# Kernel optimization log

Hardware: AMD Instinct MI355X
Metric: run time of the kernel (lower is better)

## Reference

```python
import jax, jax.numpy as jnp
import numpy as np

B, S, D_IN, D_OUT = 4, 2048, 1024, 1024


def setup_inputs() -> dict:
    key = jax.random.key(0)
    k1, k2, k3, k4 = jax.random.split(key, 4)
    x = jax.random.normal(k1, (B, S, D_IN), dtype=jnp.float32)
    # torch nn.Linear weight layout: [d_out, d_in]
    wq = jax.random.normal(k2, (D_OUT, D_IN), dtype=jnp.float32) * (1.0 / np.sqrt(D_IN))
    wk = jax.random.normal(k3, (D_OUT, D_IN), dtype=jnp.float32) * (1.0 / np.sqrt(D_IN))
    wv = jax.random.normal(k4, (D_OUT, D_IN), dtype=jnp.float32) * (1.0 / np.sqrt(D_IN))
    return {"x": x, "wq": wq, "wk": wk, "wv": wv}


def reference(x, wq, wk, wv):
    # q,k,v: [b, s, d_out]
    q = jnp.einsum('bsd,od->bso', x, wq)
    k = jnp.einsum('bsd,od->bso', x, wk)
    v = jnp.einsum('bsd,od->bso', x, wv)
    scale = 1.0 / jnp.sqrt(jnp.asarray(k.shape[-1], dtype=q.dtype))
    scores = jnp.einsum('bqd,bkd->bqk', q, k)  # [b, s, s]
    s = scores.shape[-1]
    causal = jnp.tril(jnp.ones((s, s), dtype=bool))
    scores = jnp.where(causal, scores, -jnp.inf)
    attn = jax.nn.softmax(scores * scale, axis=-1)
    # dropout p=0.0 -> identity
    return jnp.einsum('bqk,bkd->bqd', attn, v)
```

## Files before the change

### kernel.cpp

```cpp
#include <hip/hip_runtime.h>
#include <hip/hip_bf16.h>
#include <cstdint>

#define BATCH 4
#define SEQ   2048
#define DIN   1024
#define DOUT  1024
#define SCALE 0.03125f

typedef unsigned short u16;
typedef float  f32x4  __attribute__((ext_vector_type(4)));
typedef __bf16 bf16x8 __attribute__((ext_vector_type(8)));

__device__ __forceinline__ u16 f2bf(float f) {
    unsigned u = __float_as_uint(f);
    unsigned r = 0x7fffu + ((u >> 16) & 1u);
    return (u16)((u + r) >> 16);
}

__device__ __forceinline__ f32x4 mfma16(bf16x8 a, bf16x8 b, f32x4 c) {
    return __builtin_amdgcn_mfma_f32_16x16x32_bf16(a, b, c, 0, 0, 0);
}

__device__ __forceinline__ void gl_lds16(const u16* g, u16* l) {
    __builtin_amdgcn_global_load_lds(
        (const __attribute__((address_space(1))) unsigned int*)g,
        (__attribute__((address_space(3))) unsigned int*)l, 16, 0, 0);
}

#define BAR    asm volatile("s_barrier" ::: "memory")
#define VMCNT3 asm volatile("s_waitcnt vmcnt(3)" ::: "memory")
#define VMCNT8 asm volatile("s_waitcnt vmcnt(8)" ::: "memory")
#define VMCNT0 asm volatile("s_waitcnt vmcnt(0)" ::: "memory")
#define LGKM0  asm volatile("s_waitcnt lgkmcnt(0)" ::: "memory")

__global__ __launch_bounds__(256) void cvt_all(const float* __restrict__ x,
                                               const float* __restrict__ wq,
                                               const float* __restrict__ wk,
                                               const float* __restrict__ wv,
                                               u16* __restrict__ dst,
                                               float* __restrict__ rowsum) {
    const size_t NX = (size_t)BATCH * SEQ * DIN;
    size_t gt = (size_t)blockIdx.x * 256 + threadIdx.x;
    if (gt < 1024) {
        f32x4 z = {0.f, 0.f, 0.f, 0.f};
        *(f32x4*)(rowsum + gt * 8) = z;
        *(f32x4*)(rowsum + gt * 8 + 4) = z;
    }
    size_t e = gt * 8;
    const float* src;
    size_t off;
    if (e < NX) { src = x; off = e; }
    else {
        size_t r = e - NX;
        int w = (int)(r >> 20);
        src = (w == 0) ? wq : (w == 1) ? wk : wv;
        off = r & ((1u << 20) - 1);
    }
    f32x4 a = *(const f32x4*)(src + off);
    f32x4 b = *(const f32x4*)(src + off + 4);
    uint4 o;
    o.x = (unsigned)f2bf(a[0]) | ((unsigned)f2bf(a[1]) << 16);
    o.y = (unsigned)f2bf(a[2]) | ((unsigned)f2bf(a[3]) << 16);
    o.z = (unsigned)f2bf(b[0]) | ((unsigned)f2bf(b[1]) << 16);
    o.w = (unsigned)f2bf(b[2]) | ((unsigned)f2bf(b[3]) << 16);
    *(uint4*)(dst + e) = o;
}

__device__ __forceinline__ void stg128(const u16* __restrict__ g, int ld,
                                       u16* unit, int tid) {
#pragma unroll
    for (int i = 0; i < 2; i++) {
        int D = (i * 512 + tid) * 16;
        int r = D >> 7, w = D & 127;
        int gcol = (w ^ ((r & 7) << 4)) >> 1;
        gl_lds16(g + (size_t)r * ld + gcol, unit + (i * 512 + (tid >> 6) * 64) * 8);
    }
}

__device__ __forceinline__ void stg192(const u16* __restrict__ g, int ld,
                                       u16* unit, int tid) {
#pragma unroll
    for (int i = 0; i < 3; i++) {
        int D = (i * 512 + tid) * 16;
        int r = D >> 7, w = D & 127;
        int gcol = (w ^ ((r & 7) << 4)) >> 1;
        gl_lds16(g + (size_t)r * ld + gcol, unit + (i * 512 + (tid >> 6) * 64) * 8);
    }
}

__device__ __forceinline__ void stg4(const u16* __restrict__ g, int ld,
                                     u16* unit, int tid) {
#pragma unroll
    for (int i = 0; i < 4; i++) {
        int D = (i * 256 + tid) * 16;
        int r = D >> 7, w = D & 127;
        int gcol = (w ^ ((r & 7) << 4)) >> 1;
        gl_lds16(g + (size_t)r * ld + gcol, unit + (i * 256 + (tid >> 6) * 64) * 8);
    }
}

__device__ __forceinline__ void rd4(const u16* unit, int rowbase, int l15, int l4,
                                    bf16x8 f[4][2]) {
    const char* u = (const char*)unit;
#pragma unroll
    for (int i = 0; i < 4; i++) {
        int row = rowbase + i * 16 + l15;
#pragma unroll
        for (int kk = 0; kk < 2; kk++)
            f[i][kk] = *(const bf16x8*)(u + row * 128 +
                                        ((kk * 64 + l4 * 16) ^ ((row & 7) << 4)));
    }
}

__device__ __forceinline__ void rd3(const u16* unit, int rowbase, int l15, int l4,
                                    bf16x8 f[3][2]) {
    const char* u = (const char*)unit;
#pragma unroll
    for (int i = 0; i < 3; i++) {
        int row = rowbase + i * 16 + l15;
#pragma unroll
        for (int kk = 0; kk < 2; kk++)
            f[i][kk] = *(const bf16x8*)(u + row * 128 +
                                        ((kk * 64 + l4 * 16) ^ ((row & 7) << 4)));
    }
}

__device__ __forceinline__ void g4_body(u16* lds, const u16* __restrict__ Ag,
                                        int lda, const u16* __restrict__ Bg,
                                        int ldb, int nkt, int wm, int wn,
                                        int l15, int l4, int tid,
                                        f32x4 acc[4][4]) {
    bf16x8 a[4][2], b[4][2];
    u16* A0 = lds;          u16* B0 = lds + 8192;
    u16* A1 = lds + 16384;  u16* B1 = lds + 24576;
    stg4(Ag, lda, A0, tid);      stg4(Bg, ldb, B0, tid);
    stg4(Ag + 64, lda, A1, tid); stg4(Bg + 64, ldb, B1, tid);
    VMCNT8; BAR;
    for (int t = 0; t < nkt; t += 2) {
        {
            const int k2 = ((t + 2 < nkt) ? t + 2 : nkt - 1) * 64;
            rd4(A0, wm * 64, l15, l4, a);
            rd4(B0, wn * 64, l15, l4, b);
            BAR;
            __builtin_amdgcn_s_setprio(1);
#pragma unroll
            for (int kk = 0; kk < 2; kk++)
#pragma unroll
                for (int mi = 0; mi < 4; mi++)
#pragma unroll
                    for (int ni = 0; ni < 2; ni++)
                        acc[mi][ni] = mfma16(a[mi][kk], b[ni][kk], acc[mi][ni]);
            __builtin_amdgcn_s_setprio(0);
            LGKM0; BAR;
            stg4(Ag + k2, lda, A0, tid);
            stg4(Bg + k2, ldb, B0, tid);
            VMCNT8; BAR;
            __builtin_amdgcn_s_setprio(1);
#pragma unroll
            for (int kk = 0; kk < 2; kk++)
#pragma unroll
                for (int mi = 0; mi < 4; mi++)
#pragma unroll
                    for (int ni = 2; ni < 4; ni++)
                        acc[mi][ni] = mfma16(a[mi][kk], b[ni][kk], acc[mi][ni]);
            __builtin_amdgcn_s_setprio(0);
            BAR;
        }
        {
            const int k3 = ((t + 3 < nkt) ? t + 3 : nkt - 1) * 64;
            rd4(A1, wm * 64, l15, l4, a);
            rd4(B1, wn * 64, l15, l4, b);
            BAR;
            __builtin_amdgcn_s_setprio(1);
#pragma unroll
            for (int kk = 0; kk < 2; kk++)
#pragma unroll
                for (int mi = 0; mi < 4; mi++)
#pragma unroll
                    for (int ni = 0; ni < 2; ni++)
                        acc[mi][ni] = mfma16(a[mi][kk], b[ni][kk], acc[mi][ni]);
            __builtin_amdgcn_s_setprio(0);
            LGKM0; BAR;
            stg4(Ag + k3, lda, A1, tid);
            stg4(Bg + k3, ldb, B1, tid);
            VMCNT8; BAR;
            __builtin_amdgcn_s_setprio(1);
#pragma unroll
            for (int kk = 0; kk < 2; kk++)
#pragma unroll
                for (int mi = 0; mi < 4; mi++)
#pragma unroll
                    for (int ni = 2; ni < 4; ni++)
                        acc[mi][ni] = mfma16(a[mi][kk], b[ni][kk], acc[mi][ni]);
            __builtin_amdgcn_s_setprio(0);
            BAR;
        }
    }
    VMCNT0;
}

#define QKV_PH0(AU, BU, ANX0, ANX1, K1)                                      \
    rd4((AU), 0, l15, l4, a);                                                \
    rd3((BU), wn * 48, l15, l4, b);                                          \
    stg128(Ag + (K1), DIN, (ANX0), tid);                                     \
    stg128(Ag + (size_t)128 * DIN + (K1), DIN, (ANX1), tid);                 \
    BAR;                                                                     \
    __builtin_amdgcn_s_setprio(1);                                           \
    _Pragma("unroll") for (int kk = 0; kk < 2; kk++)                         \
    _Pragma("unroll") for (int mi = 0; mi < 4; mi++)                         \
    _Pragma("unroll") for (int ni = 0; ni < 3; ni++)                         \
        acc[mi][ni] = mfma16(a[mi][kk], b[ni][kk], acc[mi][ni]);             \
    __builtin_amdgcn_s_setprio(0);                                           \
    BAR;

#define QKV_PH1(AU, BCUR, K2)                                                \
    rd4((AU), 64, l15, l4, a);                                               \
    stg192(Bg + (K2), DIN, (BCUR), tid);                                     \
    VMCNT3; BAR;                                                             \
    __builtin_amdgcn_s_setprio(1);                                           \
    _Pragma("unroll") for (int kk = 0; kk < 2; kk++)                         \
    _Pragma("unroll") for (int mi = 0; mi < 4; mi++)                         \
    _Pragma("unroll") for (int ni = 0; ni < 3; ni++)                         \
        acc[4 + mi][ni] = mfma16(a[mi][kk], b[ni][kk], acc[4 + mi][ni]);     \
    __builtin_amdgcn_s_setprio(0);                                           \
    BAR;

__global__ __launch_bounds__(512) void qkv_gemm192(const u16* __restrict__ xb,
                                                   const u16* __restrict__ wb,
                                                   u16* __restrict__ qkv,
                                                   u16* __restrict__ vt) {
    extern __shared__ __align__(16) u16 lds[];
    const int tid = threadIdx.x, lane = tid & 63, wid = tid >> 6;
    const int wm = wid >> 2, wn = wid & 3;
    const int l15 = lane & 15, l4 = lane >> 4;

    u16* A00 = lds;          u16* A01 = lds + 8192;
    u16* A10 = lds + 16384;  u16* A11 = lds + 24576;
    u16* B0  = lds + 32768;  u16* B1  = lds + 45056;
    u16* Ar0 = lds + wm * 8192;
    u16* Ar1 = lds + 16384 + wm * 8192;

    for (int tile = blockIdx.x; tile < 512; tile += 256) {
        const int wg = (tile & 7) * 64 + (tile >> 3);
        const int mt = wg & 31, nt = wg >> 5;
        const int m0 = mt * 256, n0 = nt * 192;
        const u16* Ag = xb + (size_t)m0 * DIN;
        const u16* Bg = wb + (size_t)n0 * DIN;
        f32x4 acc[8][3] = {};
        bf16x8 a[4][2], b[3][2];

        stg128(Ag, DIN, A00, tid);
        stg128(Ag + (size_t)128 * DIN, DIN, A01, tid);
        stg192(Bg, DIN, B0, tid);
        stg192(Bg + 64, DIN, B1, tid);
        VMCNT3;
        BAR;

        for (int i = 0; i < 8; i++) {
            const int k1 = (2 * i + 1) * 64;
            const int k2 = ((2 * i + 2 < 16) ? 2 * i + 2 : 15) * 64;
            const int k3 = ((2 * i + 3 < 16) ? 2 * i + 3 : 15) * 64;
            QKV_PH0(Ar0, B0, A10, A11, k1)
            QKV_PH1(Ar0, B0, k2)
            QKV_PH0(Ar1, B1, A00, A01, k2)
            QKV_PH1(Ar1, B1, k3)
        }
        VMCNT0;

#pragma unroll
        for (int ai = 0; ai < 8; ai++)
#pragma unroll
            for (int bj = 0; bj < 3; bj++) {
                const int colb = n0 + wn * 48 + bj * 16;
                const int row = m0 + wm * 128 + ai * 16 + l4 * 4;
                if (colb >= 2 * DOUT) {
                    int d = colb + l15 - 2 * DOUT;
                    int batch = row >> 11, s0 = row & 2047;
                    uint2 o;
                    o.x = (unsigned)f2bf(acc[ai][bj][0]) |
                          ((unsigned)f2bf(acc[ai][bj][1]) << 16);
                    o.y = (unsigned)f2bf(acc[ai][bj][2]) |
                          ((unsigned)f2bf(acc[ai][bj][3]) << 16);
                    *(uint2*)&vt[(size_t)batch * DOUT * SEQ + (size_t)d * SEQ + s0] = o;
                } else {
                    const int wsel = colb >> 10;
                    u16* Op = qkv + (size_t)wsel * ((size_t)BATCH * SEQ * DOUT);
                    const int col = (colb & 1023) + l15;
#pragma unroll
                    for (int rr = 0; rr < 4; rr++)
                        Op[(size_t)(row + rr) * DOUT + col] = f2bf(acc[ai][bj][rr]);
                }
            }
    }
}

__global__ __launch_bounds__(256) void qk4(const u16* __restrict__ qg,
                                           const u16* __restrict__ kg,
                                           u16* __restrict__ sg,
                                           float* __restrict__ rowsum) {
    extern __shared__ __align__(16) u16 lds[];
    const int bxx = blockIdx.x, batch = blockIdx.y;
    int mt = 0, base = 0;
#pragma unroll 16
    for (int m = 0; m < 16; m++) {
        int c = m + 1;
        if (bxx < base + c) { mt = m; break; }
        base += c;
    }
    const int nt = bxx - base;
    const int m0 = mt * 128, n0 = nt * 128;
    const int tid = threadIdx.x, lane = tid & 63, wid = tid >> 6;
    const int wm = wid >> 1, wn = wid & 1;
    const int l15 = lane & 15, l4 = lane >> 4;
    const size_t bo = (size_t)batch * SEQ * DOUT;

    f32x4 acc[4][4] = {};
    g4_body(lds, qg + bo + (size_t)m0 * DOUT, DOUT,
            kg + bo + (size_t)n0 * DOUT, DOUT, 16,
            wm, wn, l15, l4, tid, acc);

    u16* Sp = sg + (size_t)batch * SEQ * SEQ;
    float* Rs = rowsum + (size_t)batch * SEQ;
#pragma unroll
    for (int ai = 0; ai < 4; ai++)
#pragma unroll
        for (int rr = 0; rr < 4; rr++) {
            int q = m0 + wm * 64 + ai * 16 + l4 * 4 + rr;
            float rp = 0.f;
#pragma unroll
            for (int bj = 0; bj < 4; bj++) {
                int kc = n0 + wn * 64 + bj * 16 + l15;
                float p = (kc <= q) ? __expf(acc[ai][bj][rr] * SCALE) : 0.f;
                rp += p;
                Sp[(size_t)q * SEQ + kc] = f2bf(p);
            }
#pragma unroll
            for (int off = 8; off >= 1; off >>= 1) rp += __shfl_xor(rp, off, 16);
            if (l15 == 0) atomicAdd(&Rs[q], rp);
        }
}

__global__ __launch_bounds__(256) void pv4(const u16* __restrict__ pg,
                                           const u16* __restrict__ vtg,
                                           const float* __restrict__ rowsum,
                                           float* __restrict__ og) {
    extern __shared__ __align__(16) u16 lds[];
    const int mt = (blockIdx.z < 2) ? (15 - (int)blockIdx.x) : (int)blockIdx.x;
    const int n0 = blockIdx.y * 128, batch = blockIdx.z;
    const int m0 = mt * 128;
    const int nkt = (mt + 1) * 2;
    const int tid = threadIdx.x, lane = tid & 63, wid = tid >> 6;
    const int wm = wid >> 1, wn = wid & 1;
    const int l15 = lane & 15, l4 = lane >> 4;
    const u16* Pb = pg + (size_t)batch * SEQ * SEQ;
    const u16* Vb = vtg + (size_t)batch * DOUT * SEQ + (size_t)n0 * SEQ;
    const float* Rs = rowsum + (size_t)batch * SEQ;
    float* Ob = og + (size_t)batch * SEQ * DOUT;

    f32x4 acc[4][4] = {};
    g4_body(lds, Pb + (size_t)m0 * SEQ, SEQ, Vb, SEQ, nkt,
            wm, wn, l15, l4, tid, acc);

#pragma unroll
    for (int ai = 0; ai < 4; ai++)
#pragma unroll
        for (int rr = 0; rr < 4; rr++) {
            int q = m0 + wm * 64 + ai * 16 + l4 * 4 + rr;
            float inv = 1.0f / Rs[q];
#pragma unroll
            for (int bj = 0; bj < 4; bj++) {
                int d = n0 + wn * 64 + bj * 16 + l15;
                Ob[(size_t)q * DOUT + d] = acc[ai][bj][rr] * inv;
            }
        }
}

extern "C" void kernel_launch(void* const* d_in, const int* in_sizes, int n_in,
                              void* d_out, int out_size, void* d_ws, size_t ws_size,
                              hipStream_t stream) {
    const float* x  = (const float*)d_in[0];
    const float* wq = (const float*)d_in[1];
    const float* wk = (const float*)d_in[2];
    const float* wv = (const float*)d_in[3];
    float* out = (float*)d_out;

    const size_t NX  = (size_t)BATCH * SEQ * DIN;
    const size_t NWT = (size_t)DOUT * DIN;
    u16* xb  = (u16*)d_ws;
    u16* wb  = xb + NX;
    u16* qkv = wb + 3 * NWT;
    u16* vt  = qkv + 3 * NX;
    u16* sb  = vt + NX;
    float* rowsum = (float*)(sb + (size_t)BATCH * SEQ * SEQ);

    cvt_all<<<(NX + 3 * NWT) / 8 / 256, 256, 0, stream>>>(x, wq, wk, wv, xb, rowsum);

    (void)hipFuncSetAttribute((const void*)qkv_gemm192,
                              hipFuncAttributeMaxDynamicSharedMemorySize, 114688);
    (void)hipFuncSetAttribute((const void*)qk4,
                              hipFuncAttributeMaxDynamicSharedMemorySize, 65536);
    (void)hipFuncSetAttribute((const void*)pv4,
                              hipFuncAttributeMaxDynamicSharedMemorySize, 65536);

    qkv_gemm192<<<dim3(256), dim3(512), 114688, stream>>>(xb, wb, qkv, vt);

    qk4<<<dim3(136, BATCH), dim3(256), 65536, stream>>>(qkv, qkv + NX, sb, rowsum);

    pv4<<<dim3(16, 8, 4), dim3(256), 65536, stream>>>(sb, vt, rowsum, out);
}
```

Baseline: 147.6 us.

## Replace 512-thread 256x192 QKV GEMM with 256-thread 128x192 double-buffered tiles

Swaps the QKV projection kernel from 512-thread workgroups computing 256x192 tiles (with split A/B staging phases) for 256-thread workgroups computing 128x192 tiles. The new kernel uses a simple two-stage double buffer over K in 80 KB of LDS, and each wave holds a 64x96 accumulator. The smaller LDS footprint and smaller blocks may let more workgroups share a CU and give finer load balance. The cost is less operand reuse per tile and a somewhat different load/compute overlap schedule.

```diff
diff --git a/kernel.cpp b/kernel.cpp
--- a/kernel.cpp
+++ b/kernel.cpp
@@ -28,11 +28,11 @@
         (__attribute__((address_space(3))) unsigned int*)l, 16, 0, 0);
 }
 
-#define BAR    asm volatile("s_barrier" ::: "memory")
-#define VMCNT3 asm volatile("s_waitcnt vmcnt(3)" ::: "memory")
-#define VMCNT8 asm volatile("s_waitcnt vmcnt(8)" ::: "memory")
-#define VMCNT0 asm volatile("s_waitcnt vmcnt(0)" ::: "memory")
-#define LGKM0  asm volatile("s_waitcnt lgkmcnt(0)" ::: "memory")
+#define BAR     asm volatile("s_barrier" ::: "memory")
+#define VMCNT8  asm volatile("s_waitcnt vmcnt(8)" ::: "memory")
+#define VMCNT10 asm volatile("s_waitcnt vmcnt(10)" ::: "memory")
+#define VMCNT0  asm volatile("s_waitcnt vmcnt(0)" ::: "memory")
+#define LGKM0   asm volatile("s_waitcnt lgkmcnt(0)" ::: "memory")
 
 __global__ __launch_bounds__(256) void cvt_all(const float* __restrict__ x,
                                                const float* __restrict__ wq,
@@ -67,32 +67,21 @@
     *(uint4*)(dst + e) = o;
 }
 
-__device__ __forceinline__ void stg128(const u16* __restrict__ g, int ld,
-                                       u16* unit, int tid) {
-#pragma unroll
-    for (int i = 0; i < 2; i++) {
-        int D = (i * 512 + tid) * 16;
+__device__ __forceinline__ void stg4(const u16* __restrict__ g, int ld,
+                                     u16* unit, int tid) {
+#pragma unroll
+    for (int i = 0; i < 4; i++) {
+        int D = (i * 256 + tid) * 16;
         int r = D >> 7, w = D & 127;
         int gcol = (w ^ ((r & 7) << 4)) >> 1;
-        gl_lds16(g + (size_t)r * ld + gcol, unit + (i * 512 + (tid >> 6) * 64) * 8);
-    }
-}
-
-__device__ __forceinline__ void stg192(const u16* __restrict__ g, int ld,
-                                       u16* unit, int tid) {
-#pragma unroll
-    for (int i = 0; i < 3; i++) {
-        int D = (i * 512 + tid) * 16;
-        int r = D >> 7, w = D & 127;
-        int gcol = (w ^ ((r & 7) << 4)) >> 1;
-        gl_lds16(g + (size_t)r * ld + gcol, unit + (i * 512 + (tid >> 6) * 64) * 8);
-    }
-}
-
-__device__ __forceinline__ void stg4(const u16* __restrict__ g, int ld,
+        gl_lds16(g + (size_t)r * ld + gcol, unit + (i * 256 + (tid >> 6) * 64) * 8);
+    }
+}
+
+__device__ __forceinline__ void stg6(const u16* __restrict__ g, int ld,
                                      u16* unit, int tid) {
 #pragma unroll
-    for (int i = 0; i < 4; i++) {
+    for (int i = 0; i < 6; i++) {
         int D = (i * 256 + tid) * 16;
         int r = D >> 7, w = D & 127;
         int gcol = (w ^ ((r & 7) << 4)) >> 1;
@@ -200,11 +189,10 @@
     VMCNT0;
 }
 
-#define QKV_PH0(AU, BU, ANX0, ANX1, K1)                                      \
-    rd4((AU), 0, l15, l4, a);                                                \
-    rd3((BU), wn * 48, l15, l4, b);                                          \
-    stg128(Ag + (K1), DIN, (ANX0), tid);                                     \
-    stg128(Ag + (size_t)128 * DIN + (K1), DIN, (ANX1), tid);                 \
+#define QKV4_TILE(AC, BC, KN)                                                \
+    rd4((AC), wm * 64, l15, l4, a);                                          \
+    rd3((BC), wn * 96, l15, l4, b);                                          \
+    rd3((BC), wn * 96 + 48, l15, l4, b + 3);                                 \
     BAR;                                                                     \
     __builtin_amdgcn_s_setprio(1);                                           \
     _Pragma("unroll") for (int kk = 0; kk < 2; kk++)                         \
@@ -212,68 +200,57 @@
     _Pragma("unroll") for (int ni = 0; ni < 3; ni++)                         \
         acc[mi][ni] = mfma16(a[mi][kk], b[ni][kk], acc[mi][ni]);             \
     __builtin_amdgcn_s_setprio(0);                                           \
-    BAR;
-
-#define QKV_PH1(AU, BCUR, K2)                                                \
-    rd4((AU), 64, l15, l4, a);                                               \
-    stg192(Bg + (K2), DIN, (BCUR), tid);                                     \
-    VMCNT3; BAR;                                                             \
+    LGKM0; BAR;                                                              \
+    stg4(Ag + (KN), DIN, (AC), tid);                                         \
+    stg6(Bg + (KN), DIN, (BC), tid);                                         \
+    VMCNT10; BAR;                                                            \
     __builtin_amdgcn_s_setprio(1);                                           \
     _Pragma("unroll") for (int kk = 0; kk < 2; kk++)                         \
     _Pragma("unroll") for (int mi = 0; mi < 4; mi++)                         \
-    _Pragma("unroll") for (int ni = 0; ni < 3; ni++)                         \
-        acc[4 + mi][ni] = mfma16(a[mi][kk], b[ni][kk], acc[4 + mi][ni]);     \
+    _Pragma("unroll") for (int ni = 3; ni < 6; ni++)                         \
+        acc[mi][ni] = mfma16(a[mi][kk], b[ni][kk], acc[mi][ni]);             \
     __builtin_amdgcn_s_setprio(0);                                           \
     BAR;
 
-__global__ __launch_bounds__(512) void qkv_gemm192(const u16* __restrict__ xb,
-                                                   const u16* __restrict__ wb,
-                                                   u16* __restrict__ qkv,
-                                                   u16* __restrict__ vt) {
+__global__ __launch_bounds__(256) void qkv4(const u16* __restrict__ xb,
+                                            const u16* __restrict__ wb,
+                                            u16* __restrict__ qkv,
+                                            u16* __restrict__ vt) {
     extern __shared__ __align__(16) u16 lds[];
     const int tid = threadIdx.x, lane = tid & 63, wid = tid >> 6;
-    const int wm = wid >> 2, wn = wid & 3;
+    const int wm = wid >> 1, wn = wid & 1;
     const int l15 = lane & 15, l4 = lane >> 4;
 
-    u16* A00 = lds;          u16* A01 = lds + 8192;
-    u16* A10 = lds + 16384;  u16* A11 = lds + 24576;
-    u16* B0  = lds + 32768;  u16* B1  = lds + 45056;
-    u16* Ar0 = lds + wm * 8192;
-    u16* Ar1 = lds + 16384 + wm * 8192;
-
-    for (int tile = blockIdx.x; tile < 512; tile += 256) {
-        const int wg = (tile & 7) * 64 + (tile >> 3);
-        const int mt = wg & 31, nt = wg >> 5;
-        const int m0 = mt * 256, n0 = nt * 192;
+    u16* A0 = lds;           u16* A1 = lds + 8192;
+    u16* B0 = lds + 16384;   u16* B1 = lds + 28672;
+
+    for (int tile = blockIdx.x; tile < 1024; tile += 512) {
+        const int wg = (tile & 7) * 128 + (tile >> 3);
+        const int mt = wg & 63, nt = wg >> 6;
+        const int m0 = mt * 128, n0 = nt * 192;
         const u16* Ag = xb + (size_t)m0 * DIN;
         const u16* Bg = wb + (size_t)n0 * DIN;
-        f32x4 acc[8][3] = {};
-        bf16x8 a[4][2], b[3][2];
-
-        stg128(Ag, DIN, A00, tid);
-        stg128(Ag + (size_t)128 * DIN, DIN, A01, tid);
-        stg192(Bg, DIN, B0, tid);
-        stg192(Bg + 64, DIN, B1, tid);
-        VMCNT3;
-        BAR;
-
-        for (int i = 0; i < 8; i++) {
-            const int k1 = (2 * i + 1) * 64;
-            const int k2 = ((2 * i + 2 < 16) ? 2 * i + 2 : 15) * 64;
-            const int k3 = ((2 * i + 3 < 16) ? 2 * i + 3 : 15) * 64;
-            QKV_PH0(Ar0, B0, A10, A11, k1)
-            QKV_PH1(Ar0, B0, k2)
-            QKV_PH0(Ar1, B1, A00, A01, k2)
-            QKV_PH1(Ar1, B1, k3)
+        f32x4 acc[4][6] = {};
+        bf16x8 a[4][2], b[6][2];
+
+        stg4(Ag, DIN, A0, tid);      stg6(Bg, DIN, B0, tid);
+        stg4(Ag + 64, DIN, A1, tid); stg6(Bg + 64, DIN, B1, tid);
+        VMCNT10; BAR;
+
+        for (int t = 0; t < 16; t += 2) {
+            const int k2 = ((t + 2 < 16) ? t + 2 : 15) * 64;
+            const int k3 = ((t + 3 < 16) ? t + 3 : 15) * 64;
+            QKV4_TILE(A0, B0, k2)
+            QKV4_TILE(A1, B1, k3)
         }
         VMCNT0;
 
 #pragma unroll
-        for (int ai = 0; ai < 8; ai++)
-#pragma unroll
-            for (int bj = 0; bj < 3; bj++) {
-                const int colb = n0 + wn * 48 + bj * 16;
-                const int row = m0 + wm * 128 + ai * 16 + l4 * 4;
+        for (int ai = 0; ai < 4; ai++)
+#pragma unroll
+            for (int bj = 0; bj < 6; bj++) {
+                const int colb = n0 + wn * 96 + bj * 16;
+                const int row = m0 + wm * 64 + ai * 16 + l4 * 4;
                 if (colb >= 2 * DOUT) {
                     int d = colb + l15 - 2 * DOUT;
                     int batch = row >> 11, s0 = row & 2047;
@@ -396,14 +373,14 @@
 
     cvt_all<<<(NX + 3 * NWT) / 8 / 256, 256, 0, stream>>>(x, wq, wk, wv, xb, rowsum);
 
-    (void)hipFuncSetAttribute((const void*)qkv_gemm192,
-                              hipFuncAttributeMaxDynamicSharedMemorySize, 114688);
+    (void)hipFuncSetAttribute((const void*)qkv4,
+                              hipFuncAttributeMaxDynamicSharedMemorySize, 81920);
     (void)hipFuncSetAttribute((const void*)qk4,
                               hipFuncAttributeMaxDynamicSharedMemorySize, 65536);
     (void)hipFuncSetAttribute((const void*)pv4,
                               hipFuncAttributeMaxDynamicSharedMemorySize, 65536);
 
-    qkv_gemm192<<<dim3(256), dim3(512), 114688, stream>>>(xb, wb, qkv, vt);
+    qkv4<<<dim3(512), dim3(256), 81920, stream>>>(xb, wb, qkv, vt);
 
     qk4<<<dim3(136, BATCH), dim3(256), 65536, stream>>>(qkv, qkv + NX, sb, rowsum);
 
```

After: 169.3 us. +14.7%, slower.
